# Kernel tuning notes

Measured on AMD Instinct MI355X. Metric: run time of the kernel, lower is better.

## Reference

```python
import jax, jax.numpy as jnp
import numpy as np

N_TREE = 200
DEPTH = 3
N_LEAF = 2 ** (DEPTH + 1) - 1      # 15 internal decision nodes
N_LEAVES = N_LEAF + 1              # 16 leaves
N_NODE = 64
BATCH = 2048
D_FEAT = 512
LR = 0.01


def _leaf_paths(depth):
    """For each of the 2^(depth+1) leaves, the internal-node index and the
    left/right bit at every level (matches the tf.gather index construction:
    bit==0 -> take p, bit==1 -> take 1-p; children of node n are 2n+1, 2n+2)."""
    L = 2 ** (depth + 1)
    nodes = np.zeros((L, depth + 1), np.int32)
    bits = np.zeros((L, depth + 1), np.int32)
    for l in range(L):
        node = 0
        for d in range(depth + 1):
            bit = (l >> (depth - d)) & 1
            nodes[l, d] = node
            bits[l, d] = bit
            node = 2 * node + 1 + bit
    return nodes, bits

_NODES, _BITS = _leaf_paths(DEPTH)


def setup_inputs() -> dict:
    key = jax.random.key(0)
    ks = jax.random.split(key, 9)
    u = lambda k, s: jax.random.uniform(k, s, jnp.float32, -0.05, 0.05)  # keras 'uniform' init
    return {
        "x": jax.random.normal(ks[0], (BATCH, D_FEAT), jnp.float32),
        "y_true": jax.random.normal(ks[1], (BATCH, 1), jnp.float32),
        "w_t": u(ks[2], (N_TREE, D_FEAT, N_NODE)),
        "b_t": u(ks[3], (N_TREE, N_NODE)),
        "w_d": u(ks[4], (N_TREE, N_NODE, N_LEAF)),
        "b_d": u(ks[5], (N_TREE, N_LEAF)),
        "w_l": u(ks[6], (N_TREE, N_LEAVES)),
        "b_l": u(ks[7], (N_TREE,)),
        "f_0": jnp.full((1,), 0.5, jnp.float32),
    }


def reference(x, y_true, w_t, b_t, w_d, b_d, w_l, b_l, f_0):
    B = x.shape[0]
    # Batched per-tree small MLP (the 200-iteration Python loop in the original).
    # Dropout is identity at inference.
    h = jax.nn.relu(jnp.einsum('bd,tdn->tbn', x, w_t) + b_t[:, None, :])        # [T,B,N_NODE]
    p = jax.nn.sigmoid(jnp.einsum('tbn,tnl->tbl', h, w_d) + b_d[:, None, :])    # [T,B,15]
    # Soft binary-tree routing: mu[t,b,leaf] = prod over path of p or (1-p).
    # This reproduces the tiled-index tf.gather construction exactly.
    pn = p[..., _NODES]                                                         # [T,B,16,DEPTH+1]
    q = jnp.where(_BITS == 1, 1.0 - pn, pn)
    mu = jnp.prod(q, axis=-1)                                                   # [T,B,16]
    # Per-tree leaf score with tanh.
    f = jnp.tanh(jnp.einsum('tbl,tl->tb', mu, w_l) + b_l[:, None])              # [T,B]
    # Sequential boosting accumulation: predict_k = f_0 + lr * sum_{i<k} f_i.
    cum = f_0 + LR * jnp.cumsum(f.T, axis=1)                                    # [B,T]
    py_x = jnp.concatenate([jnp.broadcast_to(f_0[None, :], (B, 1)), cum], axis=1)  # [B,T+1]
    return py_x
```

## Files before the change

kernel.cpp:

```cpp
#include <hip/hip_runtime.h>

#define T_TREES 200
#define BATCH   2048
#define D_FEAT  512
#define N_NODE  64
#define LR      0.01f

typedef __attribute__((__ext_vector_type__(8)))  __bf16 bf16x8;
typedef __attribute__((__ext_vector_type__(16))) float  f32x16;

__device__ __forceinline__ unsigned short f32_to_bf16(float f) {
    unsigned u = __float_as_uint(f);
    u += 0x7FFFu + ((u >> 16) & 1u);
    return (unsigned short)(u >> 16);
}

__device__ __forceinline__ void gload_lds16(const void* g, void* l) {
    __builtin_amdgcn_global_load_lds(
        (__attribute__((address_space(1))) void*)(void*)g,
        (__attribute__((address_space(3))) void*)l,
        16, 0, 0);
}

__global__ __launch_bounds__(256) void prep_all(
    const float* __restrict__ x, const float* __restrict__ w_t,
    const float* __restrict__ w_d,
    unsigned short* __restrict__ x_p, unsigned short* __restrict__ w_p,
    unsigned short* __restrict__ w_dt) {
    __shared__ float tile[64 * 65];
    int b = blockIdx.x;
    if (b < 256) {
        int mb = b >> 3, slab = b & 7;
        const float* src = x + (mb * 64) * D_FEAT + slab * 64;
        #pragma unroll
        for (int p = 0; p < 16; ++p) {
            int idx = p * 256 + threadIdx.x;
            int r = idx >> 6, c = idx & 63;
            tile[r * 65 + c] = src[r * D_FEAT + c];
        }
        __syncthreads();
        int mt = mb >> 1, mq = mb & 1;
        unsigned short* dst = x_p + mt * 65536 + slab * 8192 + mq * 512;
        #pragma unroll
        for (int p = 0; p < 2; ++p) {
            int sid = p * 256 + threadIdx.x;
            int kgl = sid >> 6;
            int r   = sid & 63;
            const float* sr = &tile[r * 65 + kgl * 8];
            bf16x8 o;
            #pragma unroll
            for (int j = 0; j < 8; ++j) o[j] = (__bf16)sr[j];
            *(bf16x8*)(dst + kgl * 1024 + r * 8) = o;
        }
    } else if (b < 1856) {
        int bb = b - 256;
        int t = bb >> 3, slab = bb & 7;
        const float* src = w_t + t * (D_FEAT * N_NODE) + slab * 64 * N_NODE;
        #pragma unroll
        for (int p = 0; p < 16; ++p) {
            int idx = p * 256 + threadIdx.x;
            int d = idx >> 6, n = idx & 63;
            tile[d * 65 + n] = src[d * N_NODE + n];
        }
        __syncthreads();
        unsigned short* dst = w_p + (t >> 1) * 65536 + slab * 8192 + (t & 1) * 512;
        #pragma unroll
        for (int p = 0; p < 2; ++p) {
            int sid = p * 256 + threadIdx.x;
            int kgl = sid >> 6;
            int n   = sid & 63;
            bf16x8 o;
            #pragma unroll
            for (int j = 0; j < 8; ++j) o[j] = (__bf16)tile[(kgl * 8 + j) * 65 + n];
            *(bf16x8*)(dst + kgl * 1024 + n * 8) = o;
        }
    } else {
        int i = (b - 1856) * 256 + threadIdx.x;
        int n = i & 63;
        int l = (i >> 6) & 31;
        int t = i >> 11;
        float v = (l < 15) ? w_d[(t * 64 + n) * 15 + l] : 0.f;
        w_dt[i] = f32_to_bf16(v);
    }
}

__global__ __launch_bounds__(256, 3) void gbdt_main(
    const unsigned short* __restrict__ x_p,
    const unsigned short* __restrict__ w_p,
    const unsigned short* __restrict__ w_dt,
    const float* __restrict__ b_t,
    const float* __restrict__ b_d,
    const float* __restrict__ w_l,
    const float* __restrict__ b_l,
    float* __restrict__ f_ws)
{
    __shared__ alignas(16) char smem[49152];
    unsigned short* Hs = (unsigned short*)smem;
    __bf16*         Hb = (__bf16*)smem;
    float*          Pf = (float*)smem;

    const int tid    = threadIdx.x;
    const int lane   = tid & 63;
    const int w      = tid >> 6;
    const int lane31 = lane & 31;
    const int kh     = lane >> 5;
    const int wm     = w >> 1;
    const int wn     = w & 1;

    const int xcd  = blockIdx.x & 7;
    const int slot = blockIdx.x >> 3;
    const int mt   = slot & 15;
    const int pj   = slot >> 4;
    const int pair = xcd * 13 + pj;
    if (pair >= 100) return;
    const int t0 = pair * 2;
    const int m0 = mt * 128;

    const char* ga = (const char*)(x_p + mt * 65536) + tid * 16;
    const char* gb = (const char*)(w_p + pair * 65536) + tid * 16;

    const int aoff = kh * 2048 + (wm * 64 + lane31) * 16;
    const int boff = 8192 + kh * 2048 + (wn * 64 + lane31) * 16;

    f32x16 acc[2][2];
    #pragma unroll
    for (int mb = 0; mb < 2; ++mb)
        #pragma unroll
        for (int nb = 0; nb < 2; ++nb)
            acc[mb][nb] = (f32x16)(0.f);

#define STAGE(cn, base) do {                                              \
        gload_lds16(ga + (cn) * 8192,        (base) + tid * 16);          \
        gload_lds16(ga + (cn) * 8192 + 4096, (base) + tid * 16 + 4096);   \
        gload_lds16(gb + (cn) * 8192,        (base) + 8192 + tid * 16);   \
        gload_lds16(gb + (cn) * 8192 + 4096, (base) + 8192 + tid * 16 + 4096); \
    } while (0)

    char* rd  = smem;
    char* rd1 = smem + 16384;
    char* rd2 = smem + 32768;

    STAGE(0, rd);
    STAGE(1, rd1);

    for (int c = 0; c < 16; ++c) {
        if (c < 15) asm volatile("s_waitcnt vmcnt(4)" ::: "memory");
        else        asm volatile("s_waitcnt vmcnt(0)" ::: "memory");
        __builtin_amdgcn_s_barrier();
        if (c < 14) STAGE(c + 2, rd2);
        __builtin_amdgcn_s_setprio(1);
        #pragma unroll
        for (int s2 = 0; s2 < 2; ++s2) {
            bf16x8 av0 = *(const bf16x8*)(rd + aoff + s2 * 4096);
            bf16x8 av1 = *(const bf16x8*)(rd + aoff + s2 * 4096 + 512);
            bf16x8 bv0 = *(const bf16x8*)(rd + boff + s2 * 4096);
            bf16x8 bv1 = *(const bf16x8*)(rd + boff + s2 * 4096 + 512);
            acc[0][0] = __builtin_amdgcn_mfma_f32_32x32x16_bf16(av0, bv0, acc[0][0], 0, 0, 0);
            acc[0][1] = __builtin_amdgcn_mfma_f32_32x32x16_bf16(av0, bv1, acc[0][1], 0, 0, 0);
            acc[1][0] = __builtin_amdgcn_mfma_f32_32x32x16_bf16(av1, bv0, acc[1][0], 0, 0, 0);
            acc[1][1] = __builtin_amdgcn_mfma_f32_32x32x16_bf16(av1, bv1, acc[1][1], 0, 0, 0);
        }
        __builtin_amdgcn_s_setprio(0);
        char* t = rd; rd = rd1; rd1 = rd2; rd2 = t;
    }

    __syncthreads();

    #pragma unroll
    for (int nb = 0; nb < 2; ++nb) {
        float btv = b_t[(t0 + wn) * 64 + nb * 32 + lane31];
        #pragma unroll
        for (int mb = 0; mb < 2; ++mb)
            #pragma unroll
            for (int r = 0; r < 16; ++r) {
                int m = wm * 64 + mb * 32 + (r & 3) + 8 * (r >> 2) + 4 * kh;
                float h = fmaxf(acc[mb][nb][r] + btv, 0.f);
                Hb[wn * 8704 + m * 68 + nb * 32 + lane31] = (__bf16)h;
            }
    }
    __syncthreads();

    f32x16 acc2[2] = { (f32x16)(0.f), (f32x16)(0.f) };
    const unsigned short* pW = w_dt + (t0 + wn) * 2048 + lane31 * 64 + kh * 8;
    __builtin_amdgcn_s_setprio(1);
    #pragma unroll
    for (int s = 0; s < 4; ++s) {
        bf16x8 bv = *(const bf16x8*)(pW + s * 16);
        #pragma unroll
        for (int i = 0; i < 2; ++i) {
            const unsigned short* pH =
                Hs + wn * 8704 + (wm * 64 + i * 32 + lane31) * 68 + s * 16 + kh * 8;
            bf16x8 av = *(const bf16x8*)pH;
            acc2[i] = __builtin_amdgcn_mfma_f32_32x32x16_bf16(av, bv, acc2[i], 0, 0, 0);
        }
    }
    __builtin_amdgcn_s_setprio(0);
    __syncthreads();

    if (lane31 < 15) {
        float bdv = b_d[(t0 + wn) * 15 + lane31];
        #pragma unroll
        for (int i = 0; i < 2; ++i)
            #pragma unroll
            for (int r = 0; r < 16; ++r) {
                int m = wm * 64 + i * 32 + (r & 3) + 8 * (r >> 2) + 4 * kh;
                float lg = acc2[i][r] + bdv;
                Pf[(wn * 128 + m) * 17 + lane31] = 1.f / (1.f + __expf(-lg));
            }
    }
    __syncthreads();

    {
        int m = tid & 127;
        int j = tid >> 7;
        int t = t0 + j;
        float pv[15];
        #pragma unroll
        for (int i = 0; i < 15; ++i) pv[i] = Pf[(j * 128 + m) * 17 + i];
        float facc = 0.f;
        #pragma unroll
        for (int leaf = 0; leaf < 16; ++leaf) {
            float mu = 1.f;
            int node = 0;
            #pragma unroll
            for (int d = 0; d < 4; ++d) {
                int bit = (leaf >> (3 - d)) & 1;
                float p = pv[node];
                mu *= bit ? (1.f - p) : p;
                node = 2 * node + 1 + bit;
            }
            facc += mu * w_l[t * 16 + leaf];
        }
        f_ws[(m0 + m) * T_TREES + t] = tanhf(facc + b_l[t]);
    }
#undef STAGE
}

__global__ __launch_bounds__(256) void scan_k(const float* __restrict__ f_ws,
                                              const float* __restrict__ f0p,
                                              float* __restrict__ out) {
    int lane = threadIdx.x & 63, wid = threadIdx.x >> 6;
    int b = blockIdx.x * 4 + wid;
    float f0 = f0p[0];
    float4 v;
    if (lane < 50) v = *(const float4*)(f_ws + b * T_TREES + lane * 4);
    else           v = make_float4(0.f, 0.f, 0.f, 0.f);
    float p0 = v.x;
    float p1 = p0 + v.y;
    float p2 = p1 + v.z;
    float p3 = p2 + v.w;
    float s = p3;
    #pragma unroll
    for (int off = 1; off < 64; off <<= 1) {
        float y = __shfl_up(s, off, 64);
        if (lane >= off) s += y;
    }
    float excl = s - p3;
    if (lane < 50) {
        float* o = out + b * (T_TREES + 1) + 1 + lane * 4;
        o[0] = f0 + LR * (excl + p0);
        o[1] = f0 + LR * (excl + p1);
        o[2] = f0 + LR * (excl + p2);
        o[3] = f0 + LR * (excl + p3);
    }
    if (lane == 0) out[b * (T_TREES + 1)] = f0;
}

extern "C" void kernel_launch(void* const* d_in, const int* in_sizes, int n_in,
                              void* d_out, int out_size, void* d_ws, size_t ws_size,
                              hipStream_t stream) {
    const float* x   = (const float*)d_in[0];
    const float* w_t = (const float*)d_in[2];
    const float* b_t = (const float*)d_in[3];
    const float* w_d = (const float*)d_in[4];
    const float* b_d = (const float*)d_in[5];
    const float* w_l = (const float*)d_in[6];
    const float* b_l = (const float*)d_in[7];
    const float* f_0 = (const float*)d_in[8];
    float* out = (float*)d_out;

    char* ws = (char*)d_ws;
    unsigned short* x_p  = (unsigned short*)(ws);
    unsigned short* w_p  = (unsigned short*)(ws + 2097152);
    unsigned short* w_dt = (unsigned short*)(ws + 15204352);
    float*          f_ws = (float*)(ws + 16023552);

    prep_all<<<3456, 256, 0, stream>>>(x, w_t, w_d, x_p, w_p, w_dt);
    gbdt_main<<<1664, 256, 0, stream>>>(x_p, w_p, w_dt, b_t, b_d, w_l, b_l, f_ws);
    scan_k<<<512, 256, 0, stream>>>(f_ws, f_0, out);
}
```

Before: 132.3 us.

## Load GEMM A-operand directly into registers and shrink LDS to raise occupancy

The x tile (A operand) is no longer staged through LDS. Each wave now prefetches its A fragments straight from global memory into registers one chunk ahead. Only the w tile (B operand) keeps the LDS triple buffer, which shrinks shared memory from 48 KB to 34 KB, and the launch bound goes from 3 to 4 blocks per CU to exploit this. The aim is to cut LDS traffic and gain occupancy, at the cost of more registers and duplicated global loads of A across the two waves that share a row block.

```diff
diff --git a/kernel.cpp b/kernel.cpp
--- a/kernel.cpp
+++ b/kernel.cpp
@@ -84,7 +84,7 @@
     }
 }
 
-__global__ __launch_bounds__(256, 3) void gbdt_main(
+__global__ __launch_bounds__(256, 4) void gbdt_main(
     const unsigned short* __restrict__ x_p,
     const unsigned short* __restrict__ w_p,
     const unsigned short* __restrict__ w_dt,
@@ -94,7 +94,7 @@
     const float* __restrict__ b_l,
     float* __restrict__ f_ws)
 {
-    __shared__ alignas(16) char smem[49152];
+    __shared__ alignas(16) char smem[34816];
     unsigned short* Hs = (unsigned short*)smem;
     __bf16*         Hb = (__bf16*)smem;
     float*          Pf = (float*)smem;
@@ -116,11 +116,10 @@
     const int t0 = pair * 2;
     const int m0 = mt * 128;
 
-    const char* ga = (const char*)(x_p + mt * 65536) + tid * 16;
+    const unsigned short* pA = x_p + mt * 65536 + kh * 1024 + (wm * 64 + lane31) * 8;
     const char* gb = (const char*)(w_p + pair * 65536) + tid * 16;
 
-    const int aoff = kh * 2048 + (wm * 64 + lane31) * 16;
-    const int boff = 8192 + kh * 2048 + (wn * 64 + lane31) * 16;
+    const int boff = kh * 2048 + (wn * 64 + lane31) * 16;
 
     f32x16 acc[2][2];
     #pragma unroll
@@ -129,39 +128,50 @@
         for (int nb = 0; nb < 2; ++nb)
             acc[mb][nb] = (f32x16)(0.f);
 
-#define STAGE(cn, base) do {                                              \
-        gload_lds16(ga + (cn) * 8192,        (base) + tid * 16);          \
-        gload_lds16(ga + (cn) * 8192 + 4096, (base) + tid * 16 + 4096);   \
-        gload_lds16(gb + (cn) * 8192,        (base) + 8192 + tid * 16);   \
-        gload_lds16(gb + (cn) * 8192 + 4096, (base) + 8192 + tid * 16 + 4096); \
+#define LOAD_A(cn, areg) do {                                      \
+        _Pragma("unroll")                                          \
+        for (int s2 = 0; s2 < 2; ++s2)                             \
+            _Pragma("unroll")                                      \
+            for (int mb = 0; mb < 2; ++mb)                         \
+                (areg)[s2 * 2 + mb] =                              \
+                    *(const bf16x8*)(pA + (cn) * 4096 + s2 * 2048 + mb * 256); \
     } while (0)
 
+#define STAGE_B(cn, base) do {                                            \
+        gload_lds16(gb + (cn) * 8192,        (base) + tid * 16);          \
+        gload_lds16(gb + (cn) * 8192 + 4096, (base) + tid * 16 + 4096);   \
+    } while (0)
+
+    bf16x8 aC[4], aN[4];
+    LOAD_A(0, aC);
+    STAGE_B(0, smem);
+    STAGE_B(1, smem + 8192);
+
     char* rd  = smem;
-    char* rd1 = smem + 16384;
-    char* rd2 = smem + 32768;
-
-    STAGE(0, rd);
-    STAGE(1, rd1);
-
+    char* rd1 = smem + 8192;
+    char* st2 = smem + 16384;
+
+    #pragma unroll
     for (int c = 0; c < 16; ++c) {
-        if (c < 15) asm volatile("s_waitcnt vmcnt(4)" ::: "memory");
+        if (c < 15) asm volatile("s_waitcnt vmcnt(2)" ::: "memory");
         else        asm volatile("s_waitcnt vmcnt(0)" ::: "memory");
         __builtin_amdgcn_s_barrier();
-        if (c < 14) STAGE(c + 2, rd2);
+        if (c < 15) LOAD_A(c + 1, aN);
+        if (c < 14) STAGE_B(c + 2, st2);
         __builtin_amdgcn_s_setprio(1);
         #pragma unroll
         for (int s2 = 0; s2 < 2; ++s2) {
-            bf16x8 av0 = *(const bf16x8*)(rd + aoff + s2 * 4096);
-            bf16x8 av1 = *(const bf16x8*)(rd + aoff + s2 * 4096 + 512);
             bf16x8 bv0 = *(const bf16x8*)(rd + boff + s2 * 4096);
             bf16x8 bv1 = *(const bf16x8*)(rd + boff + s2 * 4096 + 512);
-            acc[0][0] = __builtin_amdgcn_mfma_f32_32x32x16_bf16(av0, bv0, acc[0][0], 0, 0, 0);
-            acc[0][1] = __builtin_amdgcn_mfma_f32_32x32x16_bf16(av0, bv1, acc[0][1], 0, 0, 0);
-            acc[1][0] = __builtin_amdgcn_mfma_f32_32x32x16_bf16(av1, bv0, acc[1][0], 0, 0, 0);
-            acc[1][1] = __builtin_amdgcn_mfma_f32_32x32x16_bf16(av1, bv1, acc[1][1], 0, 0, 0);
+            acc[0][0] = __builtin_amdgcn_mfma_f32_32x32x16_bf16(aC[s2 * 2 + 0], bv0, acc[0][0], 0, 0, 0);
+            acc[0][1] = __builtin_amdgcn_mfma_f32_32x32x16_bf16(aC[s2 * 2 + 0], bv1, acc[0][1], 0, 0, 0);
+            acc[1][0] = __builtin_amdgcn_mfma_f32_32x32x16_bf16(aC[s2 * 2 + 1], bv0, acc[1][0], 0, 0, 0);
+            acc[1][1] = __builtin_amdgcn_mfma_f32_32x32x16_bf16(aC[s2 * 2 + 1], bv1, acc[1][1], 0, 0, 0);
         }
         __builtin_amdgcn_s_setprio(0);
-        char* t = rd; rd = rd1; rd1 = rd2; rd2 = t;
+        char* t = rd; rd = rd1; rd1 = st2; st2 = t;
+        #pragma unroll
+        for (int i = 0; i < 4; ++i) aC[i] = aN[i];
     }
 
     __syncthreads();
@@ -233,7 +243,8 @@
         }
         f_ws[(m0 + m) * T_TREES + t] = tanhf(facc + b_l[t]);
     }
-#undef STAGE
+#undef STAGE_B
+#undef LOAD_A
 }
 
 __global__ __launch_bounds__(256) void scan_k(const float* __restrict__ f_ws,
```

New measurement: 132.0 us. About the same (-0.2%).
